# Optimization experiments

Hardware: AMD Instinct MI355X
Metric: run time of the kernel (lower is better)

Reference implementation:

```python
import jax, jax.numpy as jnp
import numpy as np

B, S, NX, H = 4, 2048, 1024, 16
D = NX // H  # head_dim = 64
P = 512      # past kv length


def setup_inputs() -> dict:
    key = jax.random.key(0)
    ks = jax.random.split(key, 4)
    std = 0.02
    return {
        "x": jax.random.normal(ks[0], (B, S, NX), jnp.float32),
        "layer_past": jax.random.normal(ks[1], (2, B, H, P, D), jnp.float32),
        "c_attn_w": jax.random.normal(ks[2], (NX, 3 * NX), jnp.float32) * std,
        "c_attn_b": jnp.zeros((3 * NX,), jnp.float32),
        "c_proj_w": jax.random.normal(ks[3], (NX, NX), jnp.float32) * std,
        "c_proj_b": jnp.zeros((NX,), jnp.float32),
    }


def _split_heads(t):
    # [B, S, NX] -> [B, H, S, D]
    b, s, _ = t.shape
    return t.reshape(b, s, H, D).transpose(0, 2, 1, 3)


def reference(x, layer_past, c_attn_w, c_attn_b, c_proj_w, c_proj_b):
    qkv = x @ c_attn_w + c_attn_b                      # [B, S, 3*NX]
    q, k, v = jnp.split(qkv, 3, axis=2)
    q = _split_heads(q)                                # [B, H, S, D]
    k = _split_heads(k)
    v = _split_heads(v)
    past_k, past_v = layer_past[0], layer_past[1]      # [B, H, P, D]
    k = jnp.concatenate([past_k, k], axis=-2)          # [B, H, P+S, D]
    v = jnp.concatenate([past_v, v], axis=-2)
    present = jnp.stack([k, v], axis=0)                # [2, B, H, P+S, D]

    w = jnp.einsum("bhqd,bhkd->bhqk", q, k)            # [B, H, S, P+S]
    w = w / jnp.sqrt(jnp.float32(k.shape[-1]))         # scale=True
    nd, ns = w.shape[-2], w.shape[-1]
    i = jnp.arange(nd)[:, None]
    j = jnp.arange(ns)[None, :]
    b = (i >= j - ns + nd).astype(w.dtype)             # causal mask, lower-right aligned
    w = w * b - 10000.0 * (1.0 - b)
    w = jax.nn.softmax(w, axis=-1)                     # attn_dropout is identity (eval)
    a = jnp.einsum("bhqk,bhkd->bhqd", w, v)            # [B, H, S, D]
    a = a.transpose(0, 2, 1, 3).reshape(x.shape[0], x.shape[1], NX)  # merge heads
    a = a @ c_proj_w + c_proj_b                        # resid_dropout identity (eval)
    return a, present
```

## Files before the change

kernel.cpp:

```cpp
#include <hip/hip_runtime.h>

#define B_  4
#define S_  2048
#define NX_ 1024
#define H_  16
#define D_  64
#define P_  512
#define NS_ 2560
#define BHND_ ((size_t)B_*H_*NS_*D_)

#define QSCALE_ 0.18033688011112042f
#define MASKC_  -14426.950408889634f

typedef __attribute__((ext_vector_type(8))) short bf16x8;
typedef __attribute__((ext_vector_type(4))) float f32x4;
typedef __attribute__((ext_vector_type(4))) float float4v;
typedef __attribute__((ext_vector_type(4))) unsigned short ushort4v;

__device__ __forceinline__ unsigned short f2bf(float f){
  union { float f; unsigned u; } v; v.f = f;
  unsigned r = v.u + 0x7FFFu + ((v.u >> 16) & 1u);
  return (unsigned short)(r >> 16);
}

__device__ __forceinline__ void gll16(const void* g, void* l){
  __builtin_amdgcn_global_load_lds(
      (const __attribute__((address_space(1))) unsigned int*)g,
      (__attribute__((address_space(3))) unsigned int*)l, 16, 0, 0);
}

__device__ __forceinline__ void bar_nodrain(){
  __builtin_amdgcn_sched_barrier(0);
  asm volatile("s_waitcnt lgkmcnt(0)" ::: "memory");
  __builtin_amdgcn_s_barrier();
  __builtin_amdgcn_sched_barrier(0);
}


__global__ void cvt_f32_bf16(const float* __restrict__ in, unsigned short* __restrict__ out, int n4){
  for (int i = blockIdx.x*blockDim.x + threadIdx.x; i < n4; i += gridDim.x*blockDim.x){
    float4v v = ((const float4v*)in)[i];
    ushort4v u = { f2bf(v.x), f2bf(v.y), f2bf(v.z), f2bf(v.w) };
    ((ushort4v*)out)[i] = u;
  }
}

__global__ void transpose_cvt(const float* __restrict__ in, unsigned short* __restrict__ out, int K, int N){
  __shared__ float tile[32][33];
  int n0 = blockIdx.x*32, k0 = blockIdx.y*32;
  int tx = threadIdx.x & 31, ty = threadIdx.x >> 5;
  #pragma unroll
  for (int r = 0; r < 32; r += 8)
    tile[ty + r][tx] = in[(size_t)(k0 + ty + r)*N + n0 + tx];
  __syncthreads();
  #pragma unroll
  for (int r = 0; r < 32; r += 8)
    out[(size_t)(n0 + ty + r)*K + k0 + tx] = f2bf(tile[tx][ty + r]);
}

__global__ void past_kernel(const float* __restrict__ past, float* __restrict__ present){
  const int total4 = 2*B_*H_*P_*D_/4;
  for (int i = blockIdx.x*blockDim.x + threadIdx.x; i < total4; i += gridDim.x*blockDim.x){
    int d4  = i & 15;
    int pos = (i >> 4) & 511;
    int h   = (i >> 13) & 15;
    int b   = (i >> 17) & 3;
    int kv  = i >> 19;
    float4v v = ((const float4v*)past)[i];
    size_t off = (((size_t)(b*H_ + h))*NS_ + pos)*D_ + d4*4;
    ((float4v*)present)[((size_t)kv*BHND_ + off) >> 2] = v;
  }
}

template<int EPI>
__global__ __launch_bounds__(256, 2) void gemm_bf16(
    const unsigned short* __restrict__ A,
    const unsigned short* __restrict__ Bt,
    const float* __restrict__ bias,
    const int K, const int N,
    float* __restrict__ out_f32,
    unsigned short* __restrict__ out_q,
    float* __restrict__ present)
{
  __shared__ unsigned short As[128*32];
  __shared__ unsigned short Bs[128*32];
  const int bm = blockIdx.x, bn = blockIdx.y;
  const int tid = threadIdx.x, lane = tid & 63, w = tid >> 6;
  const int wr = w >> 1, wc = w & 1;
  const int g = lane >> 4, li = lane & 15;
  f32x4 acc[4][4] = {};
  const char* Ab = (const char*)A + (size_t)(bm*128)*(K*2);
  const char* Bb = (const char*)Bt + (size_t)(bn*128)*(K*2);

  for (int kt = 0; kt < K; kt += 32){
    #pragma unroll
    for (int c = 0; c < 2; ++c){
      int off = c*4096 + w*1024 + lane*16;
      int row = off >> 6, col = off & 63;
      gll16(Ab + (size_t)row*(K*2) + (size_t)kt*2 + col, (char*)As + c*4096 + w*1024);
      gll16(Bb + (size_t)row*(K*2) + (size_t)kt*2 + col, (char*)Bs + c*4096 + w*1024);
    }
    __syncthreads();
    bf16x8 af[4], bfr[4];
    #pragma unroll
    for (int mf = 0; mf < 4; ++mf)
      af[mf] = *(const bf16x8*)((const char*)As + (wr*64 + mf*16 + li)*64 + g*16);
    #pragma unroll
    for (int nf = 0; nf < 4; ++nf)
      bfr[nf] = *(const bf16x8*)((const char*)Bs + (wc*64 + nf*16 + li)*64 + g*16);
    #pragma unroll
    for (int mf = 0; mf < 4; ++mf)
      #pragma unroll
      for (int nf = 0; nf < 4; ++nf)
        acc[mf][nf] = __builtin_amdgcn_mfma_f32_16x16x32_bf16(af[mf], bfr[nf], acc[mf][nf], 0, 0, 0);
    __syncthreads();
  }

  #pragma unroll
  for (int mf = 0; mf < 4; ++mf){
    #pragma unroll
    for (int nf = 0; nf < 4; ++nf){
      int n = bn*128 + wc*64 + nf*16 + li;
      float bsv = bias[n];
      #pragma unroll
      for (int r = 0; r < 4; ++r){
        int m = bm*128 + wr*64 + mf*16 + g*4 + r;
        float v = acc[mf][nf][r] + bsv;
        if (EPI == 0){
          int b = m >> 11, sI = m & 2047;
          if (n < 1024){
            int hh = n >> 6, d = n & 63;
            out_q[(((size_t)(b*H_ + hh)*S_ + sI) << 6) + d] = f2bf(v * QSCALE_);
          } else {
            int cc = n & 1023; int hh = cc >> 6, d = cc & 63;
            size_t off = (((size_t)(b*H_ + hh)*NS_ + P_ + sI) << 6) + d;
            present[(n < 2048 ? (size_t)0 : BHND_) + off] = v;
          }
        } else {
          out_f32[(size_t)m*N + n] = v;
        }
      }
    }
  }
}

__global__ __launch_bounds__(512, 2) void attn_kernel(
    const unsigned short* __restrict__ Qb,
    const float* __restrict__ presK,
    const float* __restrict__ presV,
    unsigned short* __restrict__ Aout)
{
  __shared__ unsigned short Klds[64*64];
  __shared__ unsigned short Vt[64*72];
  __shared__ unsigned short Plds[8][32*72];

  const int bh = blockIdx.y;
  const int tid = threadIdx.x, lane = tid & 63, w = tid >> 6;
  const int g = lane >> 4, li = lane & 15;

  const int krow = tid >> 3, kq8 = tid & 7;
  const int vkvp = tid & 31, vd0 = (tid >> 5) << 2;

  const float* Kbase = presK + (((size_t)bh*NS_) << 6);
  const float* Vbase = presV + (((size_t)bh*NS_) << 6);
  const int b = bh >> 4, h = bh & 15;

  #pragma unroll 1
  for (int seg = 0; seg < 2; ++seg){
    const int qsup = seg ? (7 - blockIdx.x) : blockIdx.x;
    const int nt = 4*qsup + 12;
    const int q0w = qsup*256 + w*32;

    bf16x8 qf[2][2];
    #pragma unroll
    for (int rf = 0; rf < 2; ++rf)
      #pragma unroll
      for (int ks = 0; ks < 2; ++ks)
        qf[rf][ks] = *(const bf16x8*)(Qb + (((size_t)bh*S_ + q0w + rf*16 + li) << 6) + ks*32 + g*8);

    f32x4 o[2][4];
    float mrow[2][4], lrow[2][4];
    #pragma unroll
    for (int rf = 0; rf < 2; ++rf){
      #pragma unroll
      for (int df = 0; df < 4; ++df) o[rf][df] = (f32x4){0.f,0.f,0.f,0.f};
      #pragma unroll
      for (int r = 0; r < 4; ++r){ mrow[rf][r] = -1e30f; lrow[rf][r] = 0.f; }
    }

    float4v ka, kb2, va, vb;
    {
      const float* kp = Kbase + ((size_t)krow << 6) + kq8*8;
      ka = ((const float4v*)kp)[0]; kb2 = ((const float4v*)kp)[1];
      const float* vp = Vbase + ((size_t)(2*vkvp) << 6) + vd0;
      va = *(const float4v*)vp; vb = *(const float4v*)(vp + 64);
    }

    #pragma unroll 1
    for (int t = 0; t < nt; ++t){
      bar_nodrain();
      {
        bf16x8 kw;
        #pragma unroll
        for (int j = 0; j < 4; ++j){ kw[j] = (short)f2bf(ka[j]); kw[4+j] = (short)f2bf(kb2[j]); }
        *(bf16x8*)((char*)Klds + krow*128 + ((kq8*16) ^ ((krow & 7) << 4))) = kw;
      }
      {
        #pragma unroll
        for (int j = 0; j < 4; ++j){
          unsigned pk = (unsigned)f2bf(va[j]) | ((unsigned)f2bf(vb[j]) << 16);
          *(unsigned*)((char*)Vt + (size_t)(vd0 + j)*144 + vkvp*4) = pk;
        }
      }
      if (t + 1 < nt){
        const float* kp = Kbase + ((size_t)((t+1)*64 + krow) << 6) + kq8*8;
        ka = ((const float4v*)kp)[0]; kb2 = ((const float4v*)kp)[1];
        const float* vp = Vbase + ((size_t)((t+1)*64 + 2*vkvp) << 6) + vd0;
        va = *(const float4v*)vp; vb = *(const float4v*)(vp + 64);
      }
      bar_nodrain();

      const int kbase = t*64;
      if (kbase <= q0w + 543){
        const bool needmask = (kbase + 63) > (q0w + 512);

        f32x4 s[2][4];
        #pragma unroll
        for (int cf = 0; cf < 4; ++cf){
          int row = cf*16 + li;
          int sw = (row & 7) << 4;
          const char* kb = (const char*)Klds + row*128;
          bf16x8 bk0 = *(const bf16x8*)(kb + ((g*16) ^ sw));
          bf16x8 bk1 = *(const bf16x8*)(kb + ((64 + g*16) ^ sw));
          #pragma unroll
          for (int rf = 0; rf < 2; ++rf){
            f32x4 a0 = (f32x4){0.f,0.f,0.f,0.f};
            a0 = __builtin_amdgcn_mfma_f32_16x16x32_bf16(qf[rf][0], bk0, a0, 0, 0, 0);
            a0 = __builtin_amdgcn_mfma_f32_16x16x32_bf16(qf[rf][1], bk1, a0, 0, 0, 0);
            s[rf][cf] = a0;
          }
        }

        #pragma unroll
        for (int rf = 0; rf < 2; ++rf){
          float pm[4], al[4];
          #pragma unroll
          for (int r = 0; r < 4; ++r){
            if (needmask){
              int q = q0w + rf*16 + g*4 + r;
              int lim = q + 512 - kbase;
              #pragma unroll
              for (int cf = 0; cf < 4; ++cf){
                int kl = cf*16 + li;
                s[rf][cf][r] = (kl <= lim) ? s[rf][cf][r] : MASKC_;
              }
            }
            float mx = fmaxf(fmaxf(s[rf][0][r], s[rf][1][r]), fmaxf(s[rf][2][r], s[rf][3][r]));
            pm[r] = mx;
          }
          #pragma unroll
          for (int r = 0; r < 4; ++r){
            #pragma unroll
            for (int d2 = 1; d2 < 16; d2 <<= 1)
              pm[r] = fmaxf(pm[r], __shfl_xor(pm[r], d2, 64));
            float mn = fmaxf(mrow[rf][r], pm[r]);
            al[r] = __builtin_amdgcn_exp2f(mrow[rf][r] - mn);
            mrow[rf][r] = mn;
          }
          float rs[4] = {0.f,0.f,0.f,0.f};
          #pragma unroll
          for (int cf = 0; cf < 4; ++cf){
            #pragma unroll
            for (int r = 0; r < 4; ++r){
              float p = __builtin_amdgcn_exp2f(s[rf][cf][r] - mrow[rf][r]);
              rs[r] += p;
              Plds[w][(rf*16 + g*4 + r)*72 + cf*16 + li] = f2bf(p);
            }
          }
          #pragma unroll
          for (int r = 0; r < 4; ++r){
            #pragma unroll
            for (int d2 = 1; d2 < 16; d2 <<= 1)
              rs[r] += __shfl_xor(rs[r], d2, 64);
            lrow[rf][r] = lrow[rf][r]*al[r] + rs[r];
          }
          #pragma unroll
          for (int df = 0; df < 4; ++df)
            #pragma unroll
            for (int r = 0; r < 4; ++r)
              o[rf][df][r] *= al[r];
        }

        bf16x8 bv[4][2];
        #pragma unroll
        for (int df = 0; df < 4; ++df){
          bv[df][0] = *(const bf16x8*)(Vt + (df*16 + li)*72 + g*8);
          bv[df][1] = *(const bf16x8*)(Vt + (df*16 + li)*72 + 32 + g*8);
        }
        #pragma unroll
        for (int rf = 0; rf < 2; ++rf){
          bf16x8 pa0 = *(const bf16x8*)(Plds[w] + (rf*16 + li)*72 + g*8);
          bf16x8 pa1 = *(const bf16x8*)(Plds[w] + (rf*16 + li)*72 + 32 + g*8);
          #pragma unroll
          for (int df = 0; df < 4; ++df){
            o[rf][df] = __builtin_amdgcn_mfma_f32_16x16x32_bf16(pa0, bv[df][0], o[rf][df], 0, 0, 0);
            o[rf][df] = __builtin_amdgcn_mfma_f32_16x16x32_bf16(pa1, bv[df][1], o[rf][df], 0, 0, 0);
          }
        }
      }
    }

    #pragma unroll
    for (int rf = 0; rf < 2; ++rf){
      float inv[4];
      #pragma unroll
      for (int r = 0; r < 4; ++r) inv[r] = 1.0f / lrow[rf][r];
      #pragma unroll
      for (int df = 0; df < 4; ++df)
        #pragma unroll
        for (int r = 0; r < 4; ++r){
          int q = q0w + rf*16 + g*4 + r;
          Aout[((size_t)b*S_ + q)*NX_ + h*64 + df*16 + li] = f2bf(o[rf][df][r]*inv[r]);
        }
    }
  }
}


extern "C" void kernel_launch(void* const* d_in, const int* in_sizes, int n_in,
                              void* d_out, int out_size, void* d_ws, size_t ws_size,
                              hipStream_t stream){
  const float* x          = (const float*)d_in[0];
  const float* layer_past = (const float*)d_in[1];
  const float* c_attn_w   = (const float*)d_in[2];
  const float* c_attn_b   = (const float*)d_in[3];
  const float* c_proj_w   = (const float*)d_in[4];
  const float* c_proj_b   = (const float*)d_in[5];

  float* out = (float*)d_out;
  float* present = out + (size_t)B_*S_*NX_;
  float* presK = present;
  float* presV = present + BHND_;

  unsigned short* ws = (unsigned short*)d_ws;
  unsigned short* xb     = ws;
  unsigned short* wqkvT  = xb     + (size_t)8388608;
  unsigned short* wprojT = wqkvT  + (size_t)3145728;
  unsigned short* Qb     = wprojT + (size_t)1048576;
  unsigned short* Ab     = xb;

  cvt_f32_bf16<<<2048, 256, 0, stream>>>(x, xb, (int)(8388608/4));
  transpose_cvt<<<dim3(3072/32, 1024/32), 256, 0, stream>>>(c_attn_w, wqkvT, 1024, 3072);
  transpose_cvt<<<dim3(1024/32, 1024/32), 256, 0, stream>>>(c_proj_w, wprojT, 1024, 1024);
  past_kernel<<<2048, 256, 0, stream>>>(layer_past, present);

  gemm_bf16<0><<<dim3(64, 24), 256, 0, stream>>>(xb, wqkvT, c_attn_b, 1024, 3072,
                                                 nullptr, Qb, present);
  attn_kernel<<<dim3(4, 64), 512, 0, stream>>>(Qb, presK, presV, Ab);
  gemm_bf16<1><<<dim3(64, 8), 256, 0, stream>>>(Ab, wprojT, c_proj_b, 1024, 1024,
                                                out, nullptr, nullptr);
}
```

Baseline: 440.4 us.

## Restructure attention into smaller blocks with lazy rescale and MFMA row sums

```diff
diff --git a/kernel.cpp b/kernel.cpp
--- a/kernel.cpp
+++ b/kernel.cpp
@@ -16,11 +16,18 @@
 typedef __attribute__((ext_vector_type(4))) float f32x4;
 typedef __attribute__((ext_vector_type(4))) float float4v;
 typedef __attribute__((ext_vector_type(4))) unsigned short ushort4v;
+typedef __attribute__((ext_vector_type(4))) unsigned int u32x4;
 
 __device__ __forceinline__ unsigned short f2bf(float f){
   union { float f; unsigned u; } v; v.f = f;
   unsigned r = v.u + 0x7FFFu + ((v.u >> 16) & 1u);
   return (unsigned short)(r >> 16);
+}
+
+__device__ __forceinline__ unsigned cvtpk(float lo, float hi){
+  unsigned r;
+  asm("v_cvt_pk_bf16_f32 %0, %1, %2" : "=v"(r) : "v"(lo), "v"(hi));
+  return r;
 }
 
 __device__ __forceinline__ void gll16(const void* g, void* l){
@@ -144,7 +151,7 @@
   }
 }
 
-__global__ __launch_bounds__(512, 2) void attn_kernel(
+__global__ __launch_bounds__(256, 4) void attn_kernel(
     const unsigned short* __restrict__ Qb,
     const float* __restrict__ presK,
     const float* __restrict__ presV,
@@ -152,177 +159,193 @@
 {
   __shared__ unsigned short Klds[64*64];
   __shared__ unsigned short Vt[64*72];
-  __shared__ unsigned short Plds[8][32*72];
-
-  const int bh = blockIdx.y;
+  __shared__ unsigned short Plds[4][32*72];
+
+  const int bh = blockIdx.x;
+  const int qsup = 15 - (int)blockIdx.y;
   const int tid = threadIdx.x, lane = tid & 63, w = tid >> 6;
   const int g = lane >> 4, li = lane & 15;
-
-  const int krow = tid >> 3, kq8 = tid & 7;
-  const int vkvp = tid & 31, vd0 = (tid >> 5) << 2;
+  const int q0w = qsup*128 + w*32;
+  const int nt = 2*qsup + 10;
+
+  const int krow = tid >> 2, kq16 = tid & 3;
+  const int vslot = tid & 31, vd0 = (tid >> 5) << 3;
+  const int vkv_lo = (vslot & 15) + ((vslot >> 4) << 5);
 
   const float* Kbase = presK + (((size_t)bh*NS_) << 6);
   const float* Vbase = presV + (((size_t)bh*NS_) << 6);
   const int b = bh >> 4, h = bh & 15;
 
+  bf16x8 qf[2][2];
+  #pragma unroll
+  for (int rf = 0; rf < 2; ++rf)
+    #pragma unroll
+    for (int ks = 0; ks < 2; ++ks)
+      qf[rf][ks] = *(const bf16x8*)(Qb + (((size_t)bh*S_ + q0w + rf*16 + li) << 6) + ks*32 + g*8);
+
+  bf16x8 ones;
+  #pragma unroll
+  for (int j = 0; j < 8; ++j) ones[j] = (short)0x3F80;
+
+  f32x4 o[2][4];
+  f32x4 lacc[2];
+  float mrow[2][4];
+  #pragma unroll
+  for (int rf = 0; rf < 2; ++rf){
+    #pragma unroll
+    for (int df = 0; df < 4; ++df) o[rf][df] = (f32x4){0.f,0.f,0.f,0.f};
+    lacc[rf] = (f32x4){0.f,0.f,0.f,0.f};
+    #pragma unroll
+    for (int r = 0; r < 4; ++r) mrow[rf][r] = -1e30f;
+  }
+
+  float4v kraw[4], vraw[4];
+  {
+    const float* kp = Kbase + ((size_t)krow << 6) + kq16*16;
+    #pragma unroll
+    for (int j = 0; j < 4; ++j) kraw[j] = ((const float4v*)kp)[j];
+    const float* vl = Vbase + ((size_t)vkv_lo << 6) + vd0;
+    vraw[0] = ((const float4v*)vl)[0]; vraw[1] = ((const float4v*)vl)[1];
+    const float* vh = vl + (16 << 6);
+    vraw[2] = ((const float4v*)vh)[0]; vraw[3] = ((const float4v*)vh)[1];
+  }
+
   #pragma unroll 1
-  for (int seg = 0; seg < 2; ++seg){
-    const int qsup = seg ? (7 - blockIdx.x) : blockIdx.x;
-    const int nt = 4*qsup + 12;
-    const int q0w = qsup*256 + w*32;
-
-    bf16x8 qf[2][2];
-    #pragma unroll
-    for (int rf = 0; rf < 2; ++rf)
-      #pragma unroll
-      for (int ks = 0; ks < 2; ++ks)
-        qf[rf][ks] = *(const bf16x8*)(Qb + (((size_t)bh*S_ + q0w + rf*16 + li) << 6) + ks*32 + g*8);
-
-    f32x4 o[2][4];
-    float mrow[2][4], lrow[2][4];
-    #pragma unroll
-    for (int rf = 0; rf < 2; ++rf){
-      #pragma unroll
-      for (int df = 0; df < 4; ++df) o[rf][df] = (f32x4){0.f,0.f,0.f,0.f};
-      #pragma unroll
-      for (int r = 0; r < 4; ++r){ mrow[rf][r] = -1e30f; lrow[rf][r] = 0.f; }
-    }
-
-    float4v ka, kb2, va, vb;
+  for (int t = 0; t < nt; ++t){
+    unsigned ku[8], vu[8];
     {
-      const float* kp = Kbase + ((size_t)krow << 6) + kq8*8;
-      ka = ((const float4v*)kp)[0]; kb2 = ((const float4v*)kp)[1];
-      const float* vp = Vbase + ((size_t)(2*vkvp) << 6) + vd0;
-      va = *(const float4v*)vp; vb = *(const float4v*)(vp + 64);
-    }
-
-    #pragma unroll 1
-    for (int t = 0; t < nt; ++t){
-      bar_nodrain();
-      {
-        bf16x8 kw;
-        #pragma unroll
-        for (int j = 0; j < 4; ++j){ kw[j] = (short)f2bf(ka[j]); kw[4+j] = (short)f2bf(kb2[j]); }
-        *(bf16x8*)((char*)Klds + krow*128 + ((kq8*16) ^ ((krow & 7) << 4))) = kw;
-      }
-      {
-        #pragma unroll
-        for (int j = 0; j < 4; ++j){
-          unsigned pk = (unsigned)f2bf(va[j]) | ((unsigned)f2bf(vb[j]) << 16);
-          *(unsigned*)((char*)Vt + (size_t)(vd0 + j)*144 + vkvp*4) = pk;
-        }
-      }
-      if (t + 1 < nt){
-        const float* kp = Kbase + ((size_t)((t+1)*64 + krow) << 6) + kq8*8;
-        ka = ((const float4v*)kp)[0]; kb2 = ((const float4v*)kp)[1];
-        const float* vp = Vbase + ((size_t)((t+1)*64 + 2*vkvp) << 6) + vd0;
-        va = *(const float4v*)vp; vb = *(const float4v*)(vp + 64);
-      }
-      bar_nodrain();
-
-      const int kbase = t*64;
-      if (kbase <= q0w + 543){
-        const bool needmask = (kbase + 63) > (q0w + 512);
-
-        f32x4 s[2][4];
-        #pragma unroll
-        for (int cf = 0; cf < 4; ++cf){
-          int row = cf*16 + li;
-          int sw = (row & 7) << 4;
-          const char* kb = (const char*)Klds + row*128;
-          bf16x8 bk0 = *(const bf16x8*)(kb + ((g*16) ^ sw));
-          bf16x8 bk1 = *(const bf16x8*)(kb + ((64 + g*16) ^ sw));
+      const float* kf = (const float*)kraw;
+      #pragma unroll
+      for (int j = 0; j < 8; ++j) ku[j] = cvtpk(kf[2*j], kf[2*j+1]);
+      const float* vlo = (const float*)&vraw[0];
+      const float* vhi = (const float*)&vraw[2];
+      #pragma unroll
+      for (int j = 0; j < 8; ++j) vu[j] = cvtpk(vlo[j], vhi[j]);
+    }
+
+    bar_nodrain();
+    {
+      int sw = (krow & 7) << 4;
+      char* kb = (char*)Klds + krow*128;
+      *(u32x4*)(kb + ((kq16*32) ^ sw))      = (u32x4){ku[0],ku[1],ku[2],ku[3]};
+      *(u32x4*)(kb + ((kq16*32 + 16) ^ sw)) = (u32x4){ku[4],ku[5],ku[6],ku[7]};
+    }
+    #pragma unroll
+    for (int j = 0; j < 8; ++j)
+      *(unsigned*)((char*)Vt + (size_t)(vd0 + j)*144 + vslot*4) = vu[j];
+    if (t + 1 < nt){
+      const float* kp = Kbase + ((size_t)((t+1)*64 + krow) << 6) + kq16*16;
+      #pragma unroll
+      for (int j = 0; j < 4; ++j) kraw[j] = ((const float4v*)kp)[j];
+      const float* vl = Vbase + ((size_t)((t+1)*64 + vkv_lo) << 6) + vd0;
+      vraw[0] = ((const float4v*)vl)[0]; vraw[1] = ((const float4v*)vl)[1];
+      const float* vh = vl + (16 << 6);
+      vraw[2] = ((const float4v*)vh)[0]; vraw[3] = ((const float4v*)vh)[1];
+    }
+    bar_nodrain();
+
+    const int kbase = t*64;
+    if (kbase <= q0w + 543){
+      const bool needmask = (kbase + 63) > (q0w + 512);
+
+      f32x4 s[2][4];
+      #pragma unroll
+      for (int cf = 0; cf < 4; ++cf){
+        int row = cf*16 + li;
+        int sw = (row & 7) << 4;
+        const char* kb = (const char*)Klds + row*128;
+        bf16x8 bk0 = *(const bf16x8*)(kb + ((g*16) ^ sw));
+        bf16x8 bk1 = *(const bf16x8*)(kb + ((64 + g*16) ^ sw));
+        #pragma unroll
+        for (int rf = 0; rf < 2; ++rf){
+          f32x4 a0 = (f32x4){0.f,0.f,0.f,0.f};
+          a0 = __builtin_amdgcn_mfma_f32_16x16x32_bf16(qf[rf][0], bk0, a0, 0, 0, 0);
+          a0 = __builtin_amdgcn_mfma_f32_16x16x32_bf16(qf[rf][1], bk1, a0, 0, 0, 0);
+          s[rf][cf] = a0;
+        }
+      }
+
+      #pragma unroll
+      for (int rf = 0; rf < 2; ++rf){
+        float pm[4];
+        #pragma unroll
+        for (int r = 0; r < 4; ++r){
+          if (needmask){
+            int q = q0w + rf*16 + g*4 + r;
+            int lim = q + 512 - kbase;
+            #pragma unroll
+            for (int cf = 0; cf < 4; ++cf){
+              int kl = cf*16 + li;
+              s[rf][cf][r] = (kl <= lim) ? s[rf][cf][r] : MASKC_;
+            }
+          }
+          pm[r] = fmaxf(fmaxf(s[rf][0][r], s[rf][1][r]), fmaxf(s[rf][2][r], s[rf][3][r]));
+        }
+        #pragma unroll
+        for (int r = 0; r < 4; ++r)
           #pragma unroll
-          for (int rf = 0; rf < 2; ++rf){
-            f32x4 a0 = (f32x4){0.f,0.f,0.f,0.f};
-            a0 = __builtin_amdgcn_mfma_f32_16x16x32_bf16(qf[rf][0], bk0, a0, 0, 0, 0);
-            a0 = __builtin_amdgcn_mfma_f32_16x16x32_bf16(qf[rf][1], bk1, a0, 0, 0, 0);
-            s[rf][cf] = a0;
-          }
-        }
-
-        #pragma unroll
-        for (int rf = 0; rf < 2; ++rf){
-          float pm[4], al[4];
+          for (int d2 = 1; d2 < 16; d2 <<= 1)
+            pm[r] = fmaxf(pm[r], __shfl_xor(pm[r], d2, 64));
+
+        bool grow = (pm[0] > mrow[rf][0] + 8.f) | (pm[1] > mrow[rf][1] + 8.f) |
+                    (pm[2] > mrow[rf][2] + 8.f) | (pm[3] > mrow[rf][3] + 8.f);
+        if (__ballot(grow)){
           #pragma unroll
           for (int r = 0; r < 4; ++r){
-            if (needmask){
-              int q = q0w + rf*16 + g*4 + r;
-              int lim = q + 512 - kbase;
-              #pragma unroll
-              for (int cf = 0; cf < 4; ++cf){
-                int kl = cf*16 + li;
-                s[rf][cf][r] = (kl <= lim) ? s[rf][cf][r] : MASKC_;
-              }
-            }
-            float mx = fmaxf(fmaxf(s[rf][0][r], s[rf][1][r]), fmaxf(s[rf][2][r], s[rf][3][r]));
-            pm[r] = mx;
+            float mn = fmaxf(mrow[rf][r], pm[r]);
+            float al = __builtin_amdgcn_exp2f(mrow[rf][r] - mn);
+            mrow[rf][r] = mn;
+            #pragma unroll
+            for (int df = 0; df < 4; ++df) o[rf][df][r] *= al;
+            lacc[rf][r] *= al;
           }
-          #pragma unroll
-          for (int r = 0; r < 4; ++r){
-            #pragma unroll
-            for (int d2 = 1; d2 < 16; d2 <<= 1)
-              pm[r] = fmaxf(pm[r], __shfl_xor(pm[r], d2, 64));
-            float mn = fmaxf(mrow[rf][r], pm[r]);
-            al[r] = __builtin_amdgcn_exp2f(mrow[rf][r] - mn);
-            mrow[rf][r] = mn;
-          }
-          float rs[4] = {0.f,0.f,0.f,0.f};
-          #pragma unroll
-          for (int cf = 0; cf < 4; ++cf){
-            #pragma unroll
-            for (int r = 0; r < 4; ++r){
-              float p = __builtin_amdgcn_exp2f(s[rf][cf][r] - mrow[rf][r]);
-              rs[r] += p;
-              Plds[w][(rf*16 + g*4 + r)*72 + cf*16 + li] = f2bf(p);
-            }
-          }
-          #pragma unroll
-          for (int r = 0; r < 4; ++r){
-            #pragma unroll
-            for (int d2 = 1; d2 < 16; d2 <<= 1)
-              rs[r] += __shfl_xor(rs[r], d2, 64);
-            lrow[rf][r] = lrow[rf][r]*al[r] + rs[r];
-          }
-          #pragma unroll
-          for (int df = 0; df < 4; ++df)
-            #pragma unroll
-            for (int r = 0; r < 4; ++r)
-              o[rf][df][r] *= al[r];
-        }
-
-        bf16x8 bv[4][2];
+        }
+
+        #pragma unroll
+        for (int r = 0; r < 4; ++r){
+          float p0 = __builtin_amdgcn_exp2f(s[rf][0][r] - mrow[rf][r]);
+          float p1 = __builtin_amdgcn_exp2f(s[rf][1][r] - mrow[rf][r]);
+          float p2 = __builtin_amdgcn_exp2f(s[rf][2][r] - mrow[rf][r]);
+          float p3 = __builtin_amdgcn_exp2f(s[rf][3][r] - mrow[rf][r]);
+          char* prow = (char*)Plds[w] + (size_t)(rf*16 + g*4 + r)*144 + li*4;
+          *(unsigned*)prow        = cvtpk(p0, p1);
+          *(unsigned*)(prow + 64) = cvtpk(p2, p3);
+        }
+      }
+
+      bf16x8 bv[4][2];
+      #pragma unroll
+      for (int df = 0; df < 4; ++df){
+        bv[df][0] = *(const bf16x8*)(Vt + (df*16 + li)*72 + g*8);
+        bv[df][1] = *(const bf16x8*)(Vt + (df*16 + li)*72 + 32 + g*8);
+      }
+      #pragma unroll
+      for (int rf = 0; rf < 2; ++rf){
+        bf16x8 pa0 = *(const bf16x8*)(Plds[w] + (rf*16 + li)*72 + g*8);
+        bf16x8 pa1 = *(const bf16x8*)(Plds[w] + (rf*16 + li)*72 + 32 + g*8);
         #pragma unroll
         for (int df = 0; df < 4; ++df){
-          bv[df][0] = *(const bf16x8*)(Vt + (df*16 + li)*72 + g*8);
-          bv[df][1] = *(const bf16x8*)(Vt + (df*16 + li)*72 + 32 + g*8);
-        }
-        #pragma unroll
-        for (int rf = 0; rf < 2; ++rf){
-          bf16x8 pa0 = *(const bf16x8*)(Plds[w] + (rf*16 + li)*72 + g*8);
-          bf16x8 pa1 = *(const bf16x8*)(Plds[w] + (rf*16 + li)*72 + 32 + g*8);
-          #pragma unroll
-          for (int df = 0; df < 4; ++df){
-            o[rf][df] = __builtin_amdgcn_mfma_f32_16x16x32_bf16(pa0, bv[df][0], o[rf][df], 0, 0, 0);
-            o[rf][df] = __builtin_amdgcn_mfma_f32_16x16x32_bf16(pa1, bv[df][1], o[rf][df], 0, 0, 0);
-          }
-        }
-      }
-    }
-
-    #pragma unroll
-    for (int rf = 0; rf < 2; ++rf){
-      float inv[4];
-      #pragma unroll
-      for (int r = 0; r < 4; ++r) inv[r] = 1.0f / lrow[rf][r];
-      #pragma unroll
-      for (int df = 0; df < 4; ++df)
-        #pragma unroll
-        for (int r = 0; r < 4; ++r){
-          int q = q0w + rf*16 + g*4 + r;
-          Aout[((size_t)b*S_ + q)*NX_ + h*64 + df*16 + li] = f2bf(o[rf][df][r]*inv[r]);
-        }
-    }
+          o[rf][df] = __builtin_amdgcn_mfma_f32_16x16x32_bf16(pa0, bv[df][0], o[rf][df], 0, 0, 0);
+          o[rf][df] = __builtin_amdgcn_mfma_f32_16x16x32_bf16(pa1, bv[df][1], o[rf][df], 0, 0, 0);
+        }
+        lacc[rf] = __builtin_amdgcn_mfma_f32_16x16x32_bf16(pa0, ones, lacc[rf], 0, 0, 0);
+        lacc[rf] = __builtin_amdgcn_mfma_f32_16x16x32_bf16(pa1, ones, lacc[rf], 0, 0, 0);
+      }
+    }
+  }
+
+  #pragma unroll
+  for (int rf = 0; rf < 2; ++rf){
+    float inv[4];
+    #pragma unroll
+    for (int r = 0; r < 4; ++r) inv[r] = 1.0f / lacc[rf][r];
+    #pragma unroll
+    for (int df = 0; df < 4; ++df)
+      #pragma unroll
+      for (int r = 0; r < 4; ++r){
+        int q = q0w + rf*16 + g*4 + r;
+        Aout[((size_t)b*S_ + q)*NX_ + h*64 + df*16 + li] = f2bf(o[rf][df][r]*inv[r]);
+      }
   }
 }
 
@@ -356,7 +379,7 @@
 
   gemm_bf16<0><<<dim3(64, 24), 256, 0, stream>>>(xb, wqkvT, c_attn_b, 1024, 3072,
                                                  nullptr, Qb, present);
-  attn_kernel<<<dim3(4, 64), 512, 0, stream>>>(Qb, presK, presV, Ab);
+  attn_kernel<<<dim3(64, 16), 256, 0, stream>>>(Qb, presK, presV, Ab);
   gemm_bf16<1><<<dim3(64, 8), 256, 0, stream>>>(Ab, wprojT, c_proj_b, 1024, 1024,
                                                 out, nullptr, nullptr);
 }
```

Result: slower. 608.9 us (+38.3%).
